# Performance work log

Hardware: AMD Instinct MI355X
Metric: run time of the kernel (lower is better)

Reference implementation:

```python
import jax, jax.numpy as jnp
import numpy as np

B, F, V, D = 4096, 24, 1000, 32
RED = 8            # max(1, F // 3) SENet bottleneck
COMB = 2 * F * D   # 1536
EPS = 1e-5


def setup_inputs() -> dict:
    key = jax.random.key(0)
    ks = jax.random.split(key, 12)
    return {
        "x": jax.random.randint(ks[0], (B, F), 0, V),
        "emb_tables": jax.random.normal(ks[1], (F, V, D), jnp.float32) * 0.05,
        "lin_tables": jax.random.normal(ks[2], (F, V), jnp.float32) * 0.05,
        "bias": jnp.zeros((1,), jnp.float32),
        "se_w1": jax.random.normal(ks[3], (RED, F), jnp.float32) * 0.2,
        "se_w2": jax.random.normal(ks[4], (F, RED), jnp.float32) * 0.2,
        "bil_W": jax.random.normal(ks[5], (F, F, D, D), jnp.float32) * (1.0 / np.sqrt(D)),
        "w0": jax.random.normal(ks[6], (COMB, 1024), jnp.float32) * 0.02,
        "b0": jnp.zeros((1024,), jnp.float32),
        "g0": jnp.ones((1024,), jnp.float32),
        "be0": jnp.zeros((1024,), jnp.float32),
        "w1": jax.random.normal(ks[7], (1024, 512), jnp.float32) * 0.02,
        "b1": jnp.zeros((512,), jnp.float32),
        "g1": jnp.ones((512,), jnp.float32),
        "be1": jnp.zeros((512,), jnp.float32),
        "w2": jax.random.normal(ks[8], (512, 1), jnp.float32) * 0.02,
        "b2": jnp.zeros((1,), jnp.float32),
    }


def _bilinear_field_interaction(e, W):
    # e: [B,F,D], W: [F,F,D,D]
    # out[b,i,k] = e[b,i,k] * sum_{j != i} (W[i,j] @ e[b,j])[k]
    t = jnp.einsum('ijkl,bjl->bijk', W, e)          # [B,F,F,D]
    mask = 1.0 - jnp.eye(F, dtype=e.dtype)          # zero the i==j terms
    s = jnp.einsum('bijk,ij->bik', t, mask)         # [B,F,D]
    return e * s


def _senet(e, w1, w2):
    Z = e.mean(axis=2)                              # [B,F] squeeze
    A = jax.nn.sigmoid(jax.nn.relu(Z @ w1.T) @ w2.T)  # [B,F]
    return e * A[:, :, None]


def _bn_train(h, g, b):
    m = h.mean(axis=0)
    v = h.var(axis=0)  # biased, matches torch BN normalization
    return g * (h - m) * jax.lax.rsqrt(v + EPS) + b


def reference(x, emb_tables, lin_tables, bias, se_w1, se_w2, bil_W,
              w0, b0, g0, be0, w1, b1, g1, be1, w2, b2):
    fidx = jnp.arange(F)[None, :]                   # [1,F]
    emb = emb_tables[fidx, x]                       # [B,F,D]
    lin = lin_tables[fidx, x].sum(axis=1)           # [B] first-order term

    se_emb = _senet(emb, se_w1, se_w2)
    p = _bilinear_field_interaction(emb, bil_W)     # [B,F,D]
    q = _bilinear_field_interaction(se_emb, bil_W)  # [B,F,D]
    combined = jnp.concatenate(
        [p.reshape(B, F * D), q.reshape(B, F * D)], axis=1)  # [B,2FD]

    h = jax.nn.relu(_bn_train(combined @ w0 + b0, g0, be0))
    h = jax.nn.relu(_bn_train(h @ w1 + b1, g1, be1))
    mlp_out = (h @ w2 + b2)[:, 0]                   # [B]

    logit = lin + bias[0] + mlp_out
    return jax.nn.sigmoid(logit)                    # [B]
```

## Files before the change

kernel.cpp:

```cpp
#include <hip/hip_runtime.h>

#define B_SZ 4096
#define F_SZ 24
#define V_SZ 1000
#define D_SZ 32
#define RED  8
#define FD   768
#define COMB 1536
#define H0   1024
#define H1   512
#define EPS  1e-5f

typedef __bf16 bf16x8 __attribute__((ext_vector_type(8)));
typedef float  f32x4  __attribute__((ext_vector_type(4)));
typedef const __attribute__((address_space(1))) unsigned int* gptr_t;
typedef       __attribute__((address_space(3))) unsigned int* lptr_t;

__device__ __forceinline__ float bf2f(unsigned short u) {
    union { unsigned int i; float f; } v; v.i = ((unsigned int)u) << 16; return v.f;
}
__device__ __forceinline__ unsigned short f2bf(float f) {
    union { float f; unsigned int i; } v; v.f = f;
    unsigned int u = v.i;
    return (unsigned short)((u + 0x7FFFu + ((u >> 16) & 1u)) >> 16);
}
__device__ __forceinline__ unsigned int pack2(float a, float b) {
    return (unsigned int)f2bf(a) | ((unsigned int)f2bf(b) << 16);
}

__global__ __launch_bounds__(256) void prep_gather(
        const int* __restrict__ x, const float* __restrict__ emb,
        const float* __restrict__ lint, const float* __restrict__ sw1,
        const float* __restrict__ sw2, const float* __restrict__ bw,
        const float* __restrict__ w0, const float* __restrict__ w1,
        unsigned short* __restrict__ Xbf, unsigned short* __restrict__ Wt,
        unsigned short* __restrict__ w0t, unsigned short* __restrict__ w1t,
        float* __restrict__ lin, float* __restrict__ sums) {
    int bid = blockIdx.x;
    int tid = threadIdx.x;
    if (bid < 1024) {
        int w = tid >> 6, lane = tid & 63;
        int b = bid * 4 + w;
        __shared__ int   xi[4][F_SZ];
        __shared__ float e[4][F_SZ][D_SZ];
        __shared__ float Z[4][F_SZ];
        __shared__ float r1[4][RED];
        __shared__ float Afac[4][F_SZ];
        if (lane < F_SZ) xi[w][lane] = x[b * F_SZ + lane];
        __syncthreads();
        #pragma unroll
        for (int it = 0; it < 3; it++) {
            int idx = it * 64 + lane;
            int f = idx >> 3, k4 = (idx & 7) * 4;
            float4 v = *(const float4*)&emb[((size_t)f * V_SZ + xi[w][f]) * D_SZ + k4];
            *(float4*)&e[w][f][k4] = v;
        }
        __syncthreads();
        if (lane < F_SZ) {
            float s = 0.f;
            #pragma unroll
            for (int k = 0; k < D_SZ; k++) s += e[w][lane][k];
            Z[w][lane] = s * (1.f / D_SZ);
        }
        __syncthreads();
        if (lane < RED) {
            float s = 0.f;
            #pragma unroll
            for (int f = 0; f < F_SZ; f++) s += Z[w][f] * sw1[lane * F_SZ + f];
            r1[w][lane] = fmaxf(s, 0.f);
        }
        __syncthreads();
        if (lane < F_SZ) {
            float s = 0.f;
            #pragma unroll
            for (int r = 0; r < RED; r++) s += r1[w][r] * sw2[lane * RED + r];
            Afac[w][lane] = 1.f / (1.f + expf(-s));
        }
        __syncthreads();
        #pragma unroll
        for (int it = 0; it < 3; it++) {
            int idx = it * 64 + lane;
            int f = idx >> 3, k4 = (idx & 7) * 4;
            const float* p = &e[w][f][k4];
            uint2 u, us;
            u.x = pack2(p[0], p[1]); u.y = pack2(p[2], p[3]);
            float a = Afac[w][f];
            us.x = pack2(p[0] * a, p[1] * a); us.y = pack2(p[2] * a, p[3] * a);
            *(uint2*)&Xbf[(size_t)b * FD + idx * 4] = u;
            *(uint2*)&Xbf[(size_t)(B_SZ + b) * FD + idx * 4] = us;
        }
        float lv = (lane < F_SZ) ? lint[lane * V_SZ + xi[w][lane]] : 0.f;
        #pragma unroll
        for (int off = 32; off > 0; off >>= 1) lv += __shfl_down(lv, off);
        if (lane == 0) lin[b] = lv;
    } else if (bid < 3328) {
        int o = (bid - 1024) * 256 + tid;
        int ik = o / FD, jl = o - ik * FD;
        int i = ik >> 5, k = ik & 31, j = jl >> 5, l = jl & 31;
        Wt[o] = (i == j) ? (unsigned short)0
                         : f2bf(bw[(((size_t)i * F_SZ + j) * D_SZ + k) * D_SZ + l]);
    } else if (bid < 5376) {
        __shared__ float tile[32][33];
        const float* in; unsigned short* out; int K, N, bx, by;
        if (bid < 4864) { int t = bid - 3328; in = w0; out = w0t; K = COMB; N = H0; bx = t & 31; by = t >> 5; }
        else            { int t = bid - 4864; in = w1; out = w1t; K = H0;   N = H1; bx = t & 15; by = t >> 4; }
        int tx = tid & 31, ty = tid >> 5;
        int n0 = bx * 32, k0 = by * 32;
        #pragma unroll
        for (int r = 0; r < 32; r += 8)
            tile[ty + r][tx] = in[(size_t)(k0 + ty + r) * N + n0 + tx];
        __syncthreads();
        #pragma unroll
        for (int r = 0; r < 32; r += 8)
            out[(size_t)(n0 + ty + r) * K + k0 + tx] = f2bf(tile[tx][ty + r]);
    } else {
        int o = (bid - 5376) * 256 + tid;
        sums[o] = 0.f;
    }
}

template<int MODE, int K, int N, int TM, int TN, int GX, int GY>
__global__ __launch_bounds__(256) void mfma_gemm(
        const unsigned short* __restrict__ A,
        const unsigned short* __restrict__ Bt,
        const float* __restrict__ bias,
        const unsigned short* __restrict__ Xbf,
        unsigned short* __restrict__ Obf,
        float* __restrict__ sum, float* __restrict__ sumsq,
        const float* __restrict__ psum, const float* __restrict__ psumsq,
        const float* __restrict__ g, const float* __restrict__ be) {
    constexpr int MI = TM / 32, NI = TN / 32;
    constexpr int NSUB = 4;
    constexpr int CLD = TN + 4;
    constexpr int STAGE = (TM + TN) * 256;
    constexpr int CST   = TM * CLD * 4;
    constexpr int SMEM  = STAGE > CST ? STAGE : CST;
    __shared__ __align__(16) char smem[SMEM];
    unsigned short* Abuf = (unsigned short*)smem;
    unsigned short* Bbuf = (unsigned short*)(smem + TM * 256);
    float* Cst = (float*)smem;
    __shared__ float sc_s[MODE == 2 ? K : 1];
    __shared__ float sh_s[MODE == 2 ? K : 1];
    const int tid  = threadIdx.x;
    const int lane = tid & 63, wv = tid >> 6;
    const int wm = (wv >> 1) * (TM / 2), wn = (wv & 1) * (TN / 2);
    const int fr = lane & 15, kq = lane >> 4;
    const int bid = blockIdx.x;
    const int xcd = bid & 7, slot = bid >> 3;
    const int rowb = xcd * (GY / 8) + slot / GX;
    const int colb = slot % GX;
    const int bm = rowb * TM, bn = colb * TN;
    const int srow = tid >> 2;
    const int skc  = (tid & 3) * 8;

    if (MODE == 2) {
        #pragma unroll
        for (int q = 0; q < K / 256; q++) {
            int c = q * 256 + tid;
            float m = psum[c] * (1.f / B_SZ);
            float var = psumsq[c] * (1.f / B_SZ) - m * m;
            float rstd = rsqrtf(var + EPS);
            float sc = g[c] * rstd;
            sc_s[c] = sc;
            sh_s[c] = be[c] - m * sc;
        }
        __syncthreads();
    }

    f32x4 acc[MI][NI];
    #pragma unroll
    for (int i = 0; i < MI; i++)
        #pragma unroll
        for (int j = 0; j < NI; j++) {
            f32x4 z = {0.f, 0.f, 0.f, 0.f};
            acc[i][j] = z;
        }

    uint4 hvA[NSUB];
    if (MODE == 2) {
        #pragma unroll
        for (int s = 0; s < NSUB; s++)
            hvA[s] = *(const uint4*)&A[(size_t)(bm + srow) * K + 32 * s + skc];
    }

    for (int k0 = 0; k0 < K; k0 += 32 * NSUB) {
        if (MODE == 2) {
            #pragma unroll
            for (int s = 0; s < NSUB; s++) {
                unsigned int uu[4] = {hvA[s].x, hvA[s].y, hvA[s].z, hvA[s].w};
                unsigned int oo[4];
                #pragma unroll
                for (int q = 0; q < 4; q++) {
                    int c = k0 + 32 * s + skc + 2 * q;
                    float v0 = bf2f((unsigned short)(uu[q] & 0xFFFF)) * sc_s[c] + sh_s[c];
                    float v1 = bf2f((unsigned short)(uu[q] >> 16)) * sc_s[c + 1] + sh_s[c + 1];
                    oo[q] = pack2(fmaxf(v0, 0.f), fmaxf(v1, 0.f));
                }
                uint4 ov; ov.x = oo[0]; ov.y = oo[1]; ov.z = oo[2]; ov.w = oo[3];
                *(uint4*)&Abuf[s * TM * 32 + srow * 32 + skc] = ov;
            }
            if (k0 + 32 * NSUB < K) {
                #pragma unroll
                for (int s = 0; s < NSUB; s++)
                    hvA[s] = *(const uint4*)&A[(size_t)(bm + srow) * K + k0 + 32 * NSUB + 32 * s + skc];
            }
        } else {
            #pragma unroll
            for (int s = 0; s < NSUB; s++)
                #pragma unroll
                for (int c = 0; c < TM / 64; c++) {
                    const unsigned short* ga = A + (size_t)(bm + c * 64 + srow) * K + k0 + 32 * s + skc;
                    char* la = smem + s * TM * 64 + c * 4096 + wv * 1024;
                    __builtin_amdgcn_global_load_lds((gptr_t)ga, (lptr_t)la, 16, 0, 0);
                }
        }
        #pragma unroll
        for (int s = 0; s < NSUB; s++)
            #pragma unroll
            for (int c = 0; c < TN / 64; c++) {
                const unsigned short* gb = Bt + (size_t)(bn + c * 64 + srow) * K + k0 + 32 * s + skc;
                char* lb = smem + TM * 256 + s * TN * 64 + c * 4096 + wv * 1024;
                __builtin_amdgcn_global_load_lds((gptr_t)gb, (lptr_t)lb, 16, 0, 0);
            }
        __syncthreads();
        #pragma unroll
        for (int s = 0; s < NSUB; s++) {
            bf16x8 af[MI], bfv[NI];
            #pragma unroll
            for (int mi = 0; mi < MI; mi++)
                af[mi] = *(const bf16x8*)&Abuf[s * TM * 32 + (wm + mi * 16 + fr) * 32 + kq * 8];
            #pragma unroll
            for (int ni = 0; ni < NI; ni++)
                bfv[ni] = *(const bf16x8*)&Bbuf[s * TN * 32 + (wn + ni * 16 + fr) * 32 + kq * 8];
            #pragma unroll
            for (int mi = 0; mi < MI; mi++)
                #pragma unroll
                for (int ni = 0; ni < NI; ni++)
                    acc[mi][ni] = __builtin_amdgcn_mfma_f32_16x16x32_bf16(
                        af[mi], bfv[ni], acc[mi][ni], 0, 0, 0);
        }
        __syncthreads();
    }

    if (MODE != 0) {
        #pragma unroll
        for (int ni = 0; ni < NI; ni++) {
            int col = bn + wn + ni * 16 + fr;
            float bv = bias[col];
            float s = 0.f, ss = 0.f;
            #pragma unroll
            for (int mi = 0; mi < MI; mi++)
                #pragma unroll
                for (int r = 0; r < 4; r++) {
                    float v = acc[mi][ni][r] + bv;
                    acc[mi][ni][r] = v;
                    s += v; ss += v * v;
                }
            s  += __shfl_xor(s, 16);  s  += __shfl_xor(s, 32);
            ss += __shfl_xor(ss, 16); ss += __shfl_xor(ss, 32);
            if (kq == 0) {
                atomicAdd(&sum[col], s);
                atomicAdd(&sumsq[col], ss);
            }
        }
    }

    #pragma unroll
    for (int mi = 0; mi < MI; mi++)
        #pragma unroll
        for (int ni = 0; ni < NI; ni++) {
            int lrow = wm + mi * 16 + kq * 4;
            int lcol = wn + ni * 16 + fr;
            #pragma unroll
            for (int r = 0; r < 4; r++)
                Cst[(lrow + r) * CLD + lcol] = acc[mi][ni][r];
        }
    __syncthreads();
    #pragma unroll
    for (int ps = 0; ps < TM / 32; ps++) {
        int rl = ps * 32 + (tid >> 3);
        int cl = (tid & 7) * 8;
        float4 va = *(const float4*)&Cst[rl * CLD + cl];
        float4 vb = *(const float4*)&Cst[rl * CLD + cl + 4];
        float v[8] = {va.x, va.y, va.z, va.w, vb.x, vb.y, vb.z, vb.w};
        int grow = bm + rl, gcol = bn + cl;
        if (MODE == 0) {
            uint4 xv = *(const uint4*)&Xbf[(size_t)grow * FD + gcol];
            unsigned int xu[4] = {xv.x, xv.y, xv.z, xv.w};
            unsigned int oo[4];
            #pragma unroll
            for (int q = 0; q < 4; q++) {
                float x0 = bf2f((unsigned short)(xu[q] & 0xFFFF));
                float x1 = bf2f((unsigned short)(xu[q] >> 16));
                oo[q] = pack2(x0 * v[2 * q], x1 * v[2 * q + 1]);
            }
            uint4 ov; ov.x = oo[0]; ov.y = oo[1]; ov.z = oo[2]; ov.w = oo[3];
            size_t off = (grow < B_SZ)
                ? ((size_t)grow * COMB + gcol)
                : ((size_t)(grow - B_SZ) * COMB + FD + gcol);
            *(uint4*)&Obf[off] = ov;
        } else {
            unsigned int oo[4];
            #pragma unroll
            for (int q = 0; q < 4; q++)
                oo[q] = pack2(v[2 * q], v[2 * q + 1]);
            uint4 ov; ov.x = oo[0]; ov.y = oo[1]; ov.z = oo[2]; ov.w = oo[3];
            *(uint4*)&Obf[(size_t)grow * N + gcol] = ov;
        }
    }
}

__global__ __launch_bounds__(256) void final_k(const unsigned short* __restrict__ h1,
        const float* __restrict__ sum, const float* __restrict__ sumsq,
        const float* __restrict__ g, const float* __restrict__ be,
        const float* __restrict__ w2, const float* __restrict__ b2,
        const float* __restrict__ lin, const float* __restrict__ bias,
        float* __restrict__ out) {
    __shared__ float sc_s[H1], sh_s[H1], w2_s[H1];
    int t = threadIdx.x;
    int wv = t >> 6, lane = t & 63;
    #pragma unroll
    for (int q = 0; q < 2; q++) {
        int c = q * 256 + t;
        float m = sum[c] * (1.f / B_SZ);
        float var = sumsq[c] * (1.f / B_SZ) - m * m;
        float rstd = rsqrtf(var + EPS);
        float sc = g[c] * rstd;
        sc_s[c] = sc;
        sh_s[c] = be[c] - m * sc;
        w2_s[c] = w2[c];
    }
    __syncthreads();
    int r0 = blockIdx.x * 16;
    #pragma unroll
    for (int i = 0; i < 4; i++) {
        int row = r0 + wv * 4 + i;
        int c0 = lane * 8;
        uint4 hv = *(const uint4*)&h1[(size_t)row * H1 + c0];
        unsigned int uu[4] = {hv.x, hv.y, hv.z, hv.w};
        float acc = 0.f;
        #pragma unroll
        for (int q = 0; q < 4; q++) {
            int c = c0 + 2 * q;
            float v0 = bf2f((unsigned short)(uu[q] & 0xFFFF)) * sc_s[c] + sh_s[c];
            float v1 = bf2f((unsigned short)(uu[q] >> 16)) * sc_s[c + 1] + sh_s[c + 1];
            acc += fmaxf(v0, 0.f) * w2_s[c] + fmaxf(v1, 0.f) * w2_s[c + 1];
        }
        #pragma unroll
        for (int off = 32; off > 0; off >>= 1) acc += __shfl_down(acc, off);
        if (lane == 0) {
            float logit = lin[row] + bias[0] + acc + b2[0];
            out[row] = 1.f / (1.f + expf(-logit));
        }
    }
}

extern "C" void kernel_launch(void* const* d_in, const int* in_sizes, int n_in,
                              void* d_out, int out_size, void* d_ws, size_t ws_size,
                              hipStream_t stream) {
    const int*   x    = (const int*)d_in[0];
    const float* emb  = (const float*)d_in[1];
    const float* lint = (const float*)d_in[2];
    const float* bias = (const float*)d_in[3];
    const float* sw1  = (const float*)d_in[4];
    const float* sw2  = (const float*)d_in[5];
    const float* bw   = (const float*)d_in[6];
    const float* w0   = (const float*)d_in[7];
    const float* b0   = (const float*)d_in[8];
    const float* g0   = (const float*)d_in[9];
    const float* be0  = (const float*)d_in[10];
    const float* w1   = (const float*)d_in[11];
    const float* b1   = (const float*)d_in[12];
    const float* g1   = (const float*)d_in[13];
    const float* be1  = (const float*)d_in[14];
    const float* w2   = (const float*)d_in[15];
    const float* b2   = (const float*)d_in[16];
    float* out = (float*)d_out;

    char* p = (char*)d_ws;
    auto alloc = [&](size_t bytes) { char* r = p; p += (bytes + 255) & ~(size_t)255; return r; };

    unsigned short* Xbf  = (unsigned short*)alloc((size_t)2 * B_SZ * FD * 2);
    unsigned short* Wt   = (unsigned short*)alloc((size_t)FD * FD * 2);
    unsigned short* w0t  = (unsigned short*)alloc((size_t)H0 * COMB * 2);
    unsigned short* w1t  = (unsigned short*)alloc((size_t)H1 * H0 * 2);
    unsigned short* Cbf  = (unsigned short*)alloc((size_t)B_SZ * COMB * 2);
    unsigned short* h0bf = (unsigned short*)alloc((size_t)B_SZ * H0 * 2);
    unsigned short* h1bf = (unsigned short*)alloc((size_t)B_SZ * H1 * 2);
    float* lin = (float*)alloc(B_SZ * 4);
    float* sums = (float*)alloc((2 * H0 + 2 * H1) * 4);
    float* sum0 = sums, *sumsq0 = sums + H0, *sum1 = sums + 2 * H0, *sumsq1 = sums + 2 * H0 + H1;

    prep_gather<<<5388, 256, 0, stream>>>(x, emb, lint, sw1, sw2, bw, w0, w1,
                                          Xbf, Wt, w0t, w1t, lin, sums);

    mfma_gemm<0, FD, FD, 128, 64, 12, 64><<<768, 256, 0, stream>>>(
        Xbf, Wt, nullptr, Xbf, Cbf, nullptr, nullptr, nullptr, nullptr, nullptr, nullptr);
    mfma_gemm<1, COMB, H0, 128, 64, 16, 32><<<512, 256, 0, stream>>>(
        Cbf, w0t, b0, nullptr, h0bf, sum0, sumsq0, nullptr, nullptr, nullptr, nullptr);
    mfma_gemm<2, H0, H1, 64, 64, 8, 64><<<512, 256, 0, stream>>>(
        h0bf, w1t, b1, nullptr, h1bf, sum1, sumsq1, sum0, sumsq0, g0, be0);
    final_k<<<B_SZ / 16, 256, 0, stream>>>(h1bf, sum1, sumsq1, g1, be1,
                                           w2, b2, lin, bias, out);
}
```

Before: 160.7 us.

## Move weight transposes into first GEMM launch and retile second GEMM

The fp32-to-bf16 transposes of w0 and w1 move out of the gather kernel and into extra blocks appended to the first GEMM launch. Those blocks can then run alongside the bilinear GEMM tiles rather than before them. The second GEMM's tile also shrinks from 128x64 to 64x64, doubling its grid to 1024 blocks for better occupancy. The trade-off is that transpose blocks compete with GEMM tiles for compute units, and the smaller tiles reduce data reuse per block.

```diff
diff --git a/kernel.cpp b/kernel.cpp
--- a/kernel.cpp
+++ b/kernel.cpp
@@ -32,9 +32,7 @@
         const int* __restrict__ x, const float* __restrict__ emb,
         const float* __restrict__ lint, const float* __restrict__ sw1,
         const float* __restrict__ sw2, const float* __restrict__ bw,
-        const float* __restrict__ w0, const float* __restrict__ w1,
         unsigned short* __restrict__ Xbf, unsigned short* __restrict__ Wt,
-        unsigned short* __restrict__ w0t, unsigned short* __restrict__ w1t,
         float* __restrict__ lin, float* __restrict__ sums) {
     int bid = blockIdx.x;
     int tid = threadIdx.x;
@@ -99,22 +97,8 @@
         int i = ik >> 5, k = ik & 31, j = jl >> 5, l = jl & 31;
         Wt[o] = (i == j) ? (unsigned short)0
                          : f2bf(bw[(((size_t)i * F_SZ + j) * D_SZ + k) * D_SZ + l]);
-    } else if (bid < 5376) {
-        __shared__ float tile[32][33];
-        const float* in; unsigned short* out; int K, N, bx, by;
-        if (bid < 4864) { int t = bid - 3328; in = w0; out = w0t; K = COMB; N = H0; bx = t & 31; by = t >> 5; }
-        else            { int t = bid - 4864; in = w1; out = w1t; K = H0;   N = H1; bx = t & 15; by = t >> 4; }
-        int tx = tid & 31, ty = tid >> 5;
-        int n0 = bx * 32, k0 = by * 32;
-        #pragma unroll
-        for (int r = 0; r < 32; r += 8)
-            tile[ty + r][tx] = in[(size_t)(k0 + ty + r) * N + n0 + tx];
-        __syncthreads();
-        #pragma unroll
-        for (int r = 0; r < 32; r += 8)
-            out[(size_t)(n0 + ty + r) * K + k0 + tx] = f2bf(tile[tx][ty + r]);
     } else {
-        int o = (bid - 5376) * 256 + tid;
+        int o = (bid - 3328) * 256 + tid;
         sums[o] = 0.f;
     }
 }
@@ -128,7 +112,9 @@
         unsigned short* __restrict__ Obf,
         float* __restrict__ sum, float* __restrict__ sumsq,
         const float* __restrict__ psum, const float* __restrict__ psumsq,
-        const float* __restrict__ g, const float* __restrict__ be) {
+        const float* __restrict__ g, const float* __restrict__ be,
+        const float* __restrict__ tw0, const float* __restrict__ tw1,
+        unsigned short* __restrict__ tw0t, unsigned short* __restrict__ tw1t) {
     constexpr int MI = TM / 32, NI = TN / 32;
     constexpr int NSUB = 4;
     constexpr int CLD = TN + 4;
@@ -142,10 +128,29 @@
     __shared__ float sc_s[MODE == 2 ? K : 1];
     __shared__ float sh_s[MODE == 2 ? K : 1];
     const int tid  = threadIdx.x;
+    const int bid = blockIdx.x;
+
+    if (MODE == 0 && bid >= GX * GY) {
+        int t = bid - GX * GY;
+        const float* in; unsigned short* out; int Kt, Nt, bx, by;
+        if (t < 1536) { in = tw0; out = tw0t; Kt = COMB; Nt = H0; bx = t & 31; by = t >> 5; }
+        else { t -= 1536; in = tw1; out = tw1t; Kt = H0; Nt = H1; bx = t & 15; by = t >> 4; }
+        float (*tile)[33] = (float(*)[33])smem;
+        int tx = tid & 31, ty = tid >> 5;
+        int n0 = bx * 32, k0t = by * 32;
+        #pragma unroll
+        for (int r = 0; r < 32; r += 8)
+            tile[ty + r][tx] = in[(size_t)(k0t + ty + r) * Nt + n0 + tx];
+        __syncthreads();
+        #pragma unroll
+        for (int r = 0; r < 32; r += 8)
+            out[(size_t)(n0 + ty + r) * Kt + k0t + tx] = f2bf(tile[tx][ty + r]);
+        return;
+    }
+
     const int lane = tid & 63, wv = tid >> 6;
     const int wm = (wv >> 1) * (TM / 2), wn = (wv & 1) * (TN / 2);
     const int fr = lane & 15, kq = lane >> 4;
-    const int bid = blockIdx.x;
     const int xcd = bid & 7, slot = bid >> 3;
     const int rowb = xcd * (GY / 8) + slot / GX;
     const int colb = slot % GX;
@@ -391,15 +396,18 @@
     float* sums = (float*)alloc((2 * H0 + 2 * H1) * 4);
     float* sum0 = sums, *sumsq0 = sums + H0, *sum1 = sums + 2 * H0, *sumsq1 = sums + 2 * H0 + H1;
 
-    prep_gather<<<5388, 256, 0, stream>>>(x, emb, lint, sw1, sw2, bw, w0, w1,
-                                          Xbf, Wt, w0t, w1t, lin, sums);
-
-    mfma_gemm<0, FD, FD, 128, 64, 12, 64><<<768, 256, 0, stream>>>(
-        Xbf, Wt, nullptr, Xbf, Cbf, nullptr, nullptr, nullptr, nullptr, nullptr, nullptr);
-    mfma_gemm<1, COMB, H0, 128, 64, 16, 32><<<512, 256, 0, stream>>>(
-        Cbf, w0t, b0, nullptr, h0bf, sum0, sumsq0, nullptr, nullptr, nullptr, nullptr);
+    prep_gather<<<3340, 256, 0, stream>>>(x, emb, lint, sw1, sw2, bw,
+                                          Xbf, Wt, lin, sums);
+
+    mfma_gemm<0, FD, FD, 128, 64, 12, 64><<<768 + 2048, 256, 0, stream>>>(
+        Xbf, Wt, nullptr, Xbf, Cbf, nullptr, nullptr, nullptr, nullptr, nullptr, nullptr,
+        w0, w1, w0t, w1t);
+    mfma_gemm<1, COMB, H0, 64, 64, 16, 64><<<1024, 256, 0, stream>>>(
+        Cbf, w0t, b0, nullptr, h0bf, sum0, sumsq0, nullptr, nullptr, nullptr, nullptr,
+        nullptr, nullptr, nullptr, nullptr);
     mfma_gemm<2, H0, H1, 64, 64, 8, 64><<<512, 256, 0, stream>>>(
-        h0bf, w1t, b1, nullptr, h1bf, sum1, sumsq1, sum0, sumsq0, g0, be0);
+        h0bf, w1t, b1, nullptr, h1bf, sum1, sumsq1, sum0, sumsq0, g0, be0,
+        nullptr, nullptr, nullptr, nullptr);
     final_k<<<B_SZ / 16, 256, 0, stream>>>(h1bf, sum1, sumsq1, g1, be1,
                                            w2, b2, lin, bias, out);
 }
```

After: 164.7 us. 2.5% more time.
